# Performance work log

Measured on AMD Instinct MI355X. Metric: run time of the kernel, lower is better.

## Reference

```python
import jax, jax.numpy as jnp
import numpy as np

B, S, I = 64, 64, 20          # batch, history len, input_size
H = 1024                      # hidden_size
T = 32                        # future_seq_len
LP = 16                       # last_price_size = 4 * (I // 5)
NL = 2                        # num_layers


def setup_inputs() -> dict:
    key = jax.random.key(0)
    ks = jax.random.split(key, 14)
    s = 1.0 / np.sqrt(H)  # torch LSTM/Linear default uniform init scale
    def w(k, shape):
        return jax.random.uniform(k, shape, jnp.float32, -s, s)
    return {
        "x": jax.random.normal(ks[0], (B, S, I), jnp.float32),
        "last_price": jax.random.normal(ks[1], (B, LP), jnp.float32),
        # LSTM layer 0 (input -> hidden), gates ordered i,f,g,o as in torch
        "Wih0": w(ks[2], (4 * H, I)), "Whh0": w(ks[3], (4 * H, H)),
        "bih0": w(ks[4], (4 * H,)),   "bhh0": w(ks[5], (4 * H,)),
        # LSTM layer 1 (hidden -> hidden)
        "Wih1": w(ks[6], (4 * H, H)), "Whh1": w(ks[7], (4 * H, H)),
        "bih1": w(ks[8], (4 * H,)),   "bhh1": w(ks[9], (4 * H,)),
        # fc: Linear(H+LP -> H), ReLU, Linear(H -> I)
        "W1": w(ks[10], (H, H + LP)), "b1": w(ks[11], (H,)),
        "W2": w(ks[12], (I, H)),      "b2": w(ks[13], (I,)),
    }


def _cell(x_t, h, c, Wih, Whh, bih, bhh):
    # single LSTM cell step, torch gate order i,f,g,o
    gates = x_t @ Wih.T + h @ Whh.T + (bih + bhh)     # [B, 4H]
    i, f, g, o = jnp.split(gates, 4, axis=-1)
    c = jax.nn.sigmoid(f) * c + jax.nn.sigmoid(i) * jnp.tanh(g)
    h = jax.nn.sigmoid(o) * jnp.tanh(c)
    return h, c


def _stack_step(layers, hs, cs, inp):
    nh, nc = [], []
    for l in range(NL):
        h, c = _cell(inp, hs[l], cs[l], *layers[l])
        nh.append(h); nc.append(c)
        inp = h
    return tuple(nh), tuple(nc), inp


def _forward(x, last_price, layers, W1, b1, W2, b2):
    b = x.shape[0]
    h0 = tuple(jnp.zeros((b, H), x.dtype) for _ in range(NL))
    c0 = tuple(jnp.zeros((b, H), x.dtype) for _ in range(NL))

    def enc(carry, xt):
        hs, cs = carry
        hs, cs, _ = _stack_step(layers, hs, cs, xt)
        return (hs, cs), None

    (hs, cs), _ = jax.lax.scan(enc, (h0, c0), jnp.swapaxes(x, 0, 1))

    ngroup = I // 5  # I=20 -> %5 branch of the price update

    def dec(carry, _):
        hs, cs, cur, lp = carry
        hs, cs, top = _stack_step(layers, hs, cs, cur)
        fc_in = jnp.concatenate([top, lp], axis=1)            # [B, H+LP]
        pred = jnp.maximum(fc_in @ W1.T + b1, 0.0) @ W2.T + b2  # [B, I]
        pd = jax.lax.stop_gradient(pred)                      # torch .detach()
        # lp[:, i*4:(i+1)*4] += pd[:, i*5:i*5+4] / 100
        lp = lp + pd.reshape(b, ngroup, 5)[:, :, :4].reshape(b, ngroup * 4) / 100.0
        return (hs, cs, pd, lp), pred

    cur0 = x[:, -1, :]
    _, outs = jax.lax.scan(dec, (hs, cs, cur0, last_price), None, length=T)
    return jnp.swapaxes(outs, 0, 1)  # [B, T, I]


def reference(x, last_price, Wih0, Whh0, bih0, bhh0, Wih1, Whh1, bih1, bhh1, W1, b1, W2, b2):
    layers = [(Wih0, Whh0, bih0, bhh0), (Wih1, Whh1, bih1, bhh1)]
    return _forward(x, last_price, layers, W1, b1, W2, b2)
```

## Files before the change

### kernel.cpp

```cpp
#include <hip/hip_runtime.h>

typedef __attribute__((ext_vector_type(8))) short short8;
typedef __attribute__((ext_vector_type(4))) float float4_;
typedef unsigned long long u64;
typedef __attribute__((ext_vector_type(2))) unsigned long long u64x2;

#define AGENT __HIP_MEMORY_SCOPE_AGENT

__device__ __attribute__((aligned(4096))) unsigned long long gws_static[3702784];

__device__ __forceinline__ unsigned short f2bf(float f) {
    unsigned u = __builtin_bit_cast(unsigned, f);
    u = (u + 0x7FFFu + ((u >> 16) & 1u)) >> 16;
    return (unsigned short)u;
}
__device__ __forceinline__ float bf2f(unsigned short h) {
    unsigned u = ((unsigned)h) << 16;
    return __builtin_bit_cast(float, u);
}
__device__ __forceinline__ float sigm(float x) { return 1.0f / (1.0f + __expf(-x)); }
__device__ __forceinline__ float tanhf_(float x) {
    x = fminf(fmaxf(x, -15.0f), 15.0f);
    float e = __expf(2.0f * x);
    return (e - 1.0f) / (e + 1.0f);
}

__device__ __forceinline__ void st8_coh(unsigned short* p, unsigned long long v) {
    asm volatile("global_store_dwordx2 %0, %1, off sc0 sc1" :: "v"(p), "v"(v) : "memory");
}
__device__ __forceinline__ void st2_coh(unsigned short* p, unsigned short v) {
    asm volatile("global_store_short %0, %1, off sc0 sc1" :: "v"(p), "v"((unsigned)v) : "memory");
}

__device__ __forceinline__ void gbar_arrive(unsigned* flags, unsigned target, int blk) {
    asm volatile("s_waitcnt vmcnt(0)" ::: "memory");
    __syncthreads();
    if (threadIdx.x == 0)
        __hip_atomic_store(flags + blk * 16, target, __ATOMIC_RELAXED, AGENT);
}
__device__ __forceinline__ void gbar_wait(unsigned* flags, unsigned target) {
    while (__hip_atomic_load(flags + threadIdx.x * 16, __ATOMIC_RELAXED, AGENT) < target)
        __builtin_amdgcn_s_sleep(2);
    __syncthreads();
}
__device__ __forceinline__ void gbar(unsigned* flags, unsigned target, int blk) {
    gbar_arrive(flags, target, blk);
    gbar_wait(flags, target);
}

__device__ __forceinline__ void zero4(float4_ (&a)[4]) {
    float4_ z;
    z[0] = 0.f; z[1] = 0.f; z[2] = 0.f; z[3] = 0.f;
#pragma unroll
    for (int i = 0; i < 4; i++) a[i] = z;
}
__device__ __forceinline__ void copy4(float4_ (&d)[4], const float4_ (&s)[4]) {
#pragma unroll
    for (int i = 0; i < 4; i++) d[i] = s[i];
}

#define LD2P(dst, base, OFF) \
    asm volatile("global_load_dwordx2 %0, %1, off offset:" #OFF \
                 : "=v"(dst) : "v"(base))

#define BASES8(P, A) \
    const char* P##0 = (const char*)(A) + q * 32768 + (lane >> 4) * 1024 + (lane & 15) * 8; \
    const char* P##1 = P##0 + 4096;  const char* P##2 = P##0 + 8192; \
    const char* P##3 = P##0 + 12288; const char* P##4 = P##0 + 16384; \
    const char* P##5 = P##0 + 20480; const char* P##6 = P##0 + 24576; \
    const char* P##7 = P##0 + 28672;

#define ISSUE16P(LO, HI, LD, P, O0, O1) \
    do { LD(LO[0], P##0, O0); LD(LO[1], P##1, O0); LD(LO[2], P##2, O0); \
         LD(LO[3], P##3, O0); LD(LO[4], P##4, O0); LD(LO[5], P##5, O0); \
         LD(LO[6], P##6, O0); LD(LO[7], P##7, O0); \
         LD(HI[0], P##0, O1); LD(HI[1], P##1, O1); LD(HI[2], P##2, O1); \
         LD(HI[3], P##3, O1); LD(HI[4], P##4, O1); LD(HI[5], P##5, O1); \
         LD(HI[6], P##6, O1); LD(HI[7], P##7, O1); } while (0)

#define WAITV16(N, LO, HI) \
    asm volatile("s_waitcnt vmcnt(" #N ")" \
                 : "+v"(LO[0]), "+v"(LO[1]), "+v"(LO[2]), "+v"(LO[3]), \
                   "+v"(LO[4]), "+v"(LO[5]), "+v"(LO[6]), "+v"(LO[7]), \
                   "+v"(HI[0]), "+v"(HI[1]), "+v"(HI[2]), "+v"(HI[3]), \
                   "+v"(HI[4]), "+v"(HI[5]), "+v"(HI[6]), "+v"(HI[7]))

#define MFMA8C(LO, HI, BF, ACCI) \
    do { _Pragma("unroll") \
         for (int s_ = 0; s_ < 8; s_++) { \
             u64x2 t_; t_[0] = LO[s_]; t_[1] = HI[s_]; \
             ACCI = __builtin_amdgcn_mfma_f32_16x16x32_bf16( \
                 __builtin_bit_cast(short8, t_), BF[s_], ACCI, 0, 0, 0); } } while (0)

__device__ __forceinline__ void mm_pipe(const unsigned short* __restrict__ A,
                                        int q, int lane,
                                        const short8 (&bf)[8], float4_ (&acc)[4]) {
    BASES8(p_, A)
    u64 loA[8], hiA[8], loB[8], hiB[8];
    ISSUE16P(loA, hiA, LD2P, p_, 0, 512);
    ISSUE16P(loB, hiB, LD2P, p_, 128, 640);
    WAITV16(16, loA, hiA); MFMA8C(loA, hiA, bf, acc[0]);
    ISSUE16P(loA, hiA, LD2P, p_, 256, 768);
    WAITV16(16, loB, hiB); MFMA8C(loB, hiB, bf, acc[1]);
    ISSUE16P(loB, hiB, LD2P, p_, 384, 896);
    WAITV16(16, loA, hiA); MFMA8C(loA, hiA, bf, acc[2]);
    WAITV16(0, loB, hiB);  MFMA8C(loB, hiB, bf, acc[3]);
}

__device__ __forceinline__ void write_parts(float* gp, int q, int lane, float4_ (&acc)[4]) {
    const int col = lane & 15;
    const int rbase = (lane >> 4) * 4;
#pragma unroll
    for (int mt = 0; mt < 4; mt++)
#pragma unroll
        for (int r = 0; r < 4; r++)
            gp[(q * 64 + mt * 16 + rbase + r) * 17 + col] = acc[mt][r];
}

__device__ __forceinline__ float gsum(const float* gp, int b, int c) {
    return gp[(0 * 64 + b) * 17 + c] + gp[(1 * 64 + b) * 17 + c] +
           gp[(2 * 64 + b) * 17 + c] + gp[(3 * 64 + b) * 17 + c];
}

__device__ __forceinline__ short8 packrow(const float* __restrict__ p) {
    short8 r;
#pragma unroll
    for (int j = 0; j < 8; j++) r[j] = (short)f2bf(p[j]);
    return r;
}

__global__ void __launch_bounds__(256, 1)
lstm_core(const float* __restrict__ x, const float* __restrict__ lastp,
          const float* __restrict__ Wih0, const float* __restrict__ Whh0,
          const float* __restrict__ bih0, const float* __restrict__ bhh0,
          const float* __restrict__ Wih1, const float* __restrict__ Whh1,
          const float* __restrict__ bih1, const float* __restrict__ bhh1,
          const float* __restrict__ W1, const float* __restrict__ b1,
          const float* __restrict__ W2, const float* __restrict__ b2,
          float* __restrict__ out, unsigned char* __restrict__ wsb)
{
    const int tid = threadIdx.x;
    const int blk = blockIdx.x;
    const int lane = tid & 63;
    const int q = tid >> 6;
    const int eb = tid >> 2;
    const int eu = tid & 3;
    const int D_ = blk * 4 + eu;

    unsigned* bar   = (unsigned*)wsb;
    unsigned* flags = (unsigned*)(wsb + 8192);
    unsigned short* h0base = (unsigned short*)gws_static;
    unsigned short* h1base = h0base + (size_t)97 * 65536;
    unsigned short* relub  = h0base + (size_t)194 * 65536;

    auto h0p = [&](int g) -> unsigned short* {
        return h0base + (size_t)(g + 1) * 65536;
    };
    auto h1p = [&](int g) -> unsigned short* {
        return h1base + (size_t)(g + 1) * 65536;
    };

    __shared__ float gparts[4 * 64 * 17];
    __shared__ float xlds[2][64 * 21];
    __shared__ float wih0l[16 * 20];

    if (blk == 0) {
        __hip_atomic_store(flags + tid * 16, 0u, __ATOMIC_RELAXED, AGENT);
        __syncthreads();
        if (tid == 0)
            __hip_atomic_store(bar + 544, 0x1357BDFu, __ATOMIC_RELEASE, AGENT);
    }

    for (int i = tid; i < 1280; i += 256) {
        const int bb = i / 20, mm = i - bb * 20;
        xlds[0][bb * 21 + mm] = x[bb * 1280 + mm];
    }

    const int n_ = lane & 15;
    const int gq_ = n_ >> 2, uu_ = n_ & 3;
    const int growL = gq_ * 1024 + blk * 4 + uu_;
    const int kq = (q << 8) + ((lane >> 4) << 3);

    short8 whh0f[8], wih1f[8], whh1f[8], wfusedf[8], wfcf[8];
#pragma unroll
    for (int s = 0; s < 8; s++) {
        const int k = kq + s * 32;
        whh0f[s] = packrow(Whh0 + growL * 1024 + k);
        wih1f[s] = packrow(Wih1 + growL * 1024 + k);
        whh1f[s] = packrow(Whh1 + growL * 1024 + k);
        {
            float a8[8] = {0.f, 0.f, 0.f, 0.f, 0.f, 0.f, 0.f, 0.f};
            for (int m = 0; m < 20; m++) {
                float wv = Wih0[growL * 20 + m];
                const float* w2p = W2 + m * 1024 + k;
#pragma unroll
                for (int j = 0; j < 8; j++) a8[j] += wv * w2p[j];
            }
            short8 r;
#pragma unroll
            for (int j = 0; j < 8; j++) r[j] = (short)f2bf(a8[j]);
            wfusedf[s] = r;
        }
        {
            short8 r;
            if (n_ < 4) {
                r = packrow(W1 + (blk * 4 + n_) * 1040 + k);
            } else if (n_ < 8) {
                const int D = blk * 4 + (n_ - 4);
                float a8[8] = {0.f, 0.f, 0.f, 0.f, 0.f, 0.f, 0.f, 0.f};
                for (int g2 = 0; g2 < 16; g2++) {
                    const int m = 5 * (g2 >> 2) + (g2 & 3);
                    float wv = W1[D * 1040 + 1024 + g2] * 0.01f;
                    const float* w2p = W2 + m * 1024 + k;
#pragma unroll
                    for (int j = 0; j < 8; j++) a8[j] += wv * w2p[j];
                }
#pragma unroll
                for (int j = 0; j < 8; j++) r[j] = (short)f2bf(a8[j]);
            } else {
#pragma unroll
                for (int j = 0; j < 8; j++) r[j] = 0;
            }
            wfcf[s] = r;
        }
    }

    float bias0g[4], bias1g[4], cgv[4];
#pragma unroll
    for (int g = 0; g < 4; g++) {
        const int row = g * 1024 + D_;
        bias0g[g] = bih0[row] + bhh0[row];
        bias1g[g] = bih1[row] + bhh1[row];
        float s = 0.f;
        for (int m = 0; m < 20; m++) s += Wih0[row * 20 + m] * b2[m];
        cgv[g] = s;
    }
    const float fcb = b1[D_];
    float cbv = 0.f, ustate = 0.f;
    for (int g2 = 0; g2 < 16; g2++) {
        const float w1v = W1[D_ * 1040 + 1024 + g2];
        cbv += b2[5 * (g2 >> 2) + (g2 & 3)] * w1v * 0.01f;
        ustate += lastp[eb * 16 + g2] * w1v;
    }
    float c0v = 0.f, c1v = 0.f;

    if (tid < 16) {
        const int row = (tid >> 2) * 1024 + blk * 4 + (tid & 3);
        for (int m = 0; m < 20; m++) wih0l[tid * 20 + m] = Wih0[row * 20 + m];
    }
    if (tid < 64) {
        st8_coh(h0p(-1) + blk * 256 + tid * 4, 0ull);
        st8_coh(h1p(-1) + blk * 256 + tid * 4, 0ull);
    }

    if (tid == 0) {
        while (__hip_atomic_load(bar + 544, __ATOMIC_RELAXED, AGENT) != 0x1357BDFu)
            __builtin_amdgcn_s_sleep(2);
    }
    __syncthreads();
    unsigned tgt = 1;
    gbar(flags, tgt, blk); tgt++;

    auto publish = [&](unsigned short* dst, unsigned short val) {
        st2_coh(dst + blk * 256 + tid, val);
    };

    auto l0_finish = [&](float4_ (&acc)[4], unsigned short* h0dst, int xt, int pf) {
        write_parts(gparts, q, lane, acc);
        __syncthreads();
        if (pf >= 0) {
            for (int i = tid; i < 1280; i += 256) {
                const int bb = i / 20, mm = i - bb * 20;
                xlds[pf & 1][bb * 21 + mm] = x[bb * 1280 + pf * 20 + mm];
            }
        }
        float gv[4];
#pragma unroll
        for (int g = 0; g < 4; g++) gv[g] = gsum(gparts, eb, g * 4 + eu) + bias0g[g];
        if (xt >= 0) {
#pragma unroll
            for (int g = 0; g < 4; g++) {
                float s = 0.f;
                const float* wr = &wih0l[(g * 4 + eu) * 20];
                const float* xr = &xlds[xt & 1][eb * 21];
                for (int m = 0; m < 20; m++) s += xr[m] * wr[m];
                gv[g] += s;
            }
        } else {
#pragma unroll
            for (int g = 0; g < 4; g++) gv[g] += cgv[g];
        }
        const float iv = sigm(gv[0]), fv = sigm(gv[1]);
        const float gt = tanhf_(gv[2]), ov = sigm(gv[3]);
        c0v = fv * c0v + iv * gt;
        publish(h0dst, f2bf(ov * tanhf_(c0v)));
    };

    auto l1_finish = [&](float4_ (&acc)[4], unsigned short* h1dst) {
        write_parts(gparts, q, lane, acc);
        __syncthreads();
        float gv[4];
#pragma unroll
        for (int g = 0; g < 4; g++) gv[g] = gsum(gparts, eb, g * 4 + eu) + bias1g[g];
        const float iv = sigm(gv[0]), fv = sigm(gv[1]);
        const float gt = tanhf_(gv[2]), ov = sigm(gv[3]);
        c1v = fv * c1v + iv * gt;
        publish(h1dst, f2bf(ov * tanhf_(c1v)));
    };

    auto fc_finish = [&](int t, float4_ (&acc1)[4], float4_ (&acc2)[4]) {
        const int col = lane & 15;
        const int rbase = (lane >> 4) * 4;
        if (col < 8) {
#pragma unroll
            for (int mt = 0; mt < 4; mt++)
#pragma unroll
                for (int r = 0; r < 4; r++) {
                    const float v = (col < 4) ? acc1[mt][r] : acc2[mt][r];
                    gparts[(q * 64 + mt * 16 + rbase + r) * 17 + col] = v;
                }
        }
        __syncthreads();
        const float s1 = gsum(gparts, eb, eu);
        if (t > 0) ustate += gsum(gparts, eb, 4 + eu) + cbv;
        const float rv = fmaxf(s1 + ustate + fcb, 0.f);
        publish(relub + t * 65536, f2bf(rv));
    };

    for (int g = 0; g < 64; g++) {
        float4_ acc[4];
        zero4(acc);
        mm_pipe(h0p(g - 1), q, lane, whh0f, acc);
        l0_finish(acc, h0p(g), g, (g < 63) ? g + 1 : -1);
        gbar(flags, tgt, blk); tgt++;
        zero4(acc);
        mm_pipe(h0p(g), q, lane, wih1f, acc);
        mm_pipe(h1p(g - 1), q, lane, whh1f, acc);
        l1_finish(acc, h1p(g));
    }

    float4_ haccL0[4];
    float4_ hacc2[4];
    bool haveL0 = false;
    for (int t = 0; t < 32; t++) {
        const int g = 64 + t;
        unsigned short* rp = (t > 0) ? (relub + (t - 1) * 65536) : nullptr;

        float4_ acc[4];
        if (haveL0) {
            copy4(acc, haccL0);
        } else {
            zero4(acc);
            mm_pipe(h0p(g - 1), q, lane, whh0f, acc);
        }
        if (rp) mm_pipe(rp, q, lane, wfusedf, acc);
        l0_finish(acc, h0p(g), (t == 0) ? 63 : -1, -1);
        gbar_arrive(flags, tgt, blk);
        if (rp) {
            zero4(hacc2);
            mm_pipe(rp, q, lane, wfcf, hacc2);
        }
        gbar_wait(flags, tgt); tgt++;

        zero4(acc);
        mm_pipe(h0p(g), q, lane, wih1f, acc);
        mm_pipe(h1p(g - 1), q, lane, whh1f, acc);
        l1_finish(acc, h1p(g));
        gbar_arrive(flags, tgt, blk);
        gbar_wait(flags, tgt); tgt++;

        float4_ acc1[4], acc2[4];
        zero4(acc1);
        mm_pipe(h1p(g), q, lane, wfcf, acc1);
        if (rp) copy4(acc2, hacc2); else zero4(acc2);
        fc_finish(t, acc1, acc2);
        gbar_arrive(flags, tgt, blk);
        if (t < 31) {
            zero4(haccL0);
            mm_pipe(h0p(g), q, lane, whh0f, haccL0);
            haveL0 = true;
        }
        gbar_wait(flags, tgt); tgt++;
    }

    {
        const int pj = tid >> 5;
        const int m = tid & 31;
        if (m < 20) {
            const int pidx = blk * 8 + pj;
            const int tt = pidx >> 6, bb = pidx & 63;
            const unsigned short* rr = relub + tt * 65536;
            const float* w = W2 + m * 1024;
            float acc = 0.f;
            for (int c = 0; c < 256; c++) {
                const u64 v8 = *(const u64*)(rr + c * 256 + bb * 4);
#pragma unroll
                for (int j = 0; j < 4; j++)
                    acc += bf2f((unsigned short)(v8 >> (16 * j))) * w[c * 4 + j];
            }
            out[bb * 640 + tt * 20 + m] = acc + b2[m];
        }
    }
}

extern "C" void kernel_launch(void* const* d_in, const int* in_sizes, int n_in,
                              void* d_out, int out_size, void* d_ws, size_t ws_size,
                              hipStream_t stream) {
    (void)in_sizes; (void)n_in; (void)out_size; (void)ws_size;
    const float* x     = (const float*)d_in[0];
    const float* lastp = (const float*)d_in[1];
    const float* Wih0  = (const float*)d_in[2];
    const float* Whh0  = (const float*)d_in[3];
    const float* bih0  = (const float*)d_in[4];
    const float* bhh0  = (const float*)d_in[5];
    const float* Wih1  = (const float*)d_in[6];
    const float* Whh1  = (const float*)d_in[7];
    const float* bih1  = (const float*)d_in[8];
    const float* bhh1  = (const float*)d_in[9];
    const float* W1    = (const float*)d_in[10];
    const float* b1    = (const float*)d_in[11];
    const float* W2    = (const float*)d_in[12];
    const float* b2    = (const float*)d_in[13];
    float* out = (float*)d_out;
    unsigned char* ws = (unsigned char*)d_ws;

    void* args[] = {&x, &lastp, &Wih0, &Whh0, &bih0, &bhh0, &Wih1, &Whh1,
                    &bih1, &bhh1, &W1, &b1, &W2, &b2, &out, &ws};
    hipError_t err = hipLaunchCooperativeKernel((const void*)lstm_core,
                                                dim3(256), dim3(256), args, 0, stream);
    if (err != hipSuccess) {
        hipLaunchKernelGGL(lstm_core, dim3(256), dim3(256), 0, stream,
                           x, lastp, Wih0, Whh0, bih0, bhh0, Wih1, Whh1,
                           bih1, bhh1, W1, b1, W2, b2, out, ws);
    }
}
```

Baseline: 1.439 ms.

## Halve block count, give each block 8 hidden units with dual-B MFMA

```diff
diff --git a/kernel.cpp b/kernel.cpp
--- a/kernel.cpp
+++ b/kernel.cpp
@@ -2,8 +2,8 @@
 
 typedef __attribute__((ext_vector_type(8))) short short8;
 typedef __attribute__((ext_vector_type(4))) float float4_;
+typedef __attribute__((ext_vector_type(4))) int int4_;
 typedef unsigned long long u64;
-typedef __attribute__((ext_vector_type(2))) unsigned long long u64x2;
 
 #define AGENT __HIP_MEMORY_SCOPE_AGENT
 
@@ -28,8 +28,8 @@
 __device__ __forceinline__ void st8_coh(unsigned short* p, unsigned long long v) {
     asm volatile("global_store_dwordx2 %0, %1, off sc0 sc1" :: "v"(p), "v"(v) : "memory");
 }
-__device__ __forceinline__ void st2_coh(unsigned short* p, unsigned short v) {
-    asm volatile("global_store_short %0, %1, off sc0 sc1" :: "v"(p), "v"((unsigned)v) : "memory");
+__device__ __forceinline__ void st4_coh(unsigned short* p, unsigned v) {
+    asm volatile("global_store_dword %0, %1, off sc0 sc1" :: "v"(p), "v"(v) : "memory");
 }
 
 __device__ __forceinline__ void gbar_arrive(unsigned* flags, unsigned target, int blk) {
@@ -39,8 +39,10 @@
         __hip_atomic_store(flags + blk * 16, target, __ATOMIC_RELAXED, AGENT);
 }
 __device__ __forceinline__ void gbar_wait(unsigned* flags, unsigned target) {
-    while (__hip_atomic_load(flags + threadIdx.x * 16, __ATOMIC_RELAXED, AGENT) < target)
-        __builtin_amdgcn_s_sleep(2);
+    if (threadIdx.x < 128) {
+        while (__hip_atomic_load(flags + threadIdx.x * 16, __ATOMIC_RELAXED, AGENT) < target)
+            __builtin_amdgcn_s_sleep(2);
+    }
     __syncthreads();
 }
 __device__ __forceinline__ void gbar(unsigned* flags, unsigned target, int blk) {
@@ -54,72 +56,67 @@
 #pragma unroll
     for (int i = 0; i < 4; i++) a[i] = z;
 }
-__device__ __forceinline__ void copy4(float4_ (&d)[4], const float4_ (&s)[4]) {
-#pragma unroll
-    for (int i = 0; i < 4; i++) d[i] = s[i];
-}
-
-#define LD2P(dst, base, OFF) \
-    asm volatile("global_load_dwordx2 %0, %1, off offset:" #OFF \
+
+#define LD4P(dst, base, OFF) \
+    asm volatile("global_load_dwordx4 %0, %1, off offset:" #OFF \
                  : "=v"(dst) : "v"(base))
 
 #define BASES8(P, A) \
-    const char* P##0 = (const char*)(A) + q * 32768 + (lane >> 4) * 1024 + (lane & 15) * 8; \
+    const char* P##0 = (const char*)(A) + q * 32768 + (lane >> 4) * 1024 + (lane & 15) * 16; \
     const char* P##1 = P##0 + 4096;  const char* P##2 = P##0 + 8192; \
     const char* P##3 = P##0 + 12288; const char* P##4 = P##0 + 16384; \
     const char* P##5 = P##0 + 20480; const char* P##6 = P##0 + 24576; \
     const char* P##7 = P##0 + 28672;
 
-#define ISSUE16P(LO, HI, LD, P, O0, O1) \
-    do { LD(LO[0], P##0, O0); LD(LO[1], P##1, O0); LD(LO[2], P##2, O0); \
-         LD(LO[3], P##3, O0); LD(LO[4], P##4, O0); LD(LO[5], P##5, O0); \
-         LD(LO[6], P##6, O0); LD(LO[7], P##7, O0); \
-         LD(HI[0], P##0, O1); LD(HI[1], P##1, O1); LD(HI[2], P##2, O1); \
-         LD(HI[3], P##3, O1); LD(HI[4], P##4, O1); LD(HI[5], P##5, O1); \
-         LD(HI[6], P##6, O1); LD(HI[7], P##7, O1); } while (0)
-
-#define WAITV16(N, LO, HI) \
+#define ISSUE8(F, P, OFF) \
+    do { LD4P(F[0], P##0, OFF); LD4P(F[1], P##1, OFF); LD4P(F[2], P##2, OFF); \
+         LD4P(F[3], P##3, OFF); LD4P(F[4], P##4, OFF); LD4P(F[5], P##5, OFF); \
+         LD4P(F[6], P##6, OFF); LD4P(F[7], P##7, OFF); } while (0)
+
+#define WAITV8(N, F) \
     asm volatile("s_waitcnt vmcnt(" #N ")" \
-                 : "+v"(LO[0]), "+v"(LO[1]), "+v"(LO[2]), "+v"(LO[3]), \
-                   "+v"(LO[4]), "+v"(LO[5]), "+v"(LO[6]), "+v"(LO[7]), \
-                   "+v"(HI[0]), "+v"(HI[1]), "+v"(HI[2]), "+v"(HI[3]), \
-                   "+v"(HI[4]), "+v"(HI[5]), "+v"(HI[6]), "+v"(HI[7]))
-
-#define MFMA8C(LO, HI, BF, ACCI) \
+                 : "+v"(F[0]), "+v"(F[1]), "+v"(F[2]), "+v"(F[3]), \
+                   "+v"(F[4]), "+v"(F[5]), "+v"(F[6]), "+v"(F[7]))
+
+#define MFMA8D(F, B1, B2, A1, A2) \
     do { _Pragma("unroll") \
          for (int s_ = 0; s_ < 8; s_++) { \
-             u64x2 t_; t_[0] = LO[s_]; t_[1] = HI[s_]; \
-             ACCI = __builtin_amdgcn_mfma_f32_16x16x32_bf16( \
-                 __builtin_bit_cast(short8, t_), BF[s_], ACCI, 0, 0, 0); } } while (0)
+             short8 f_ = __builtin_bit_cast(short8, F[s_]); \
+             A1 = __builtin_amdgcn_mfma_f32_16x16x32_bf16(f_, B1[s_], A1, 0, 0, 0); \
+             A2 = __builtin_amdgcn_mfma_f32_16x16x32_bf16(f_, B2[s_], A2, 0, 0, 0); } } while (0)
 
 __device__ __forceinline__ void mm_pipe(const unsigned short* __restrict__ A,
                                         int q, int lane,
-                                        const short8 (&bf)[8], float4_ (&acc)[4]) {
+                                        const short8 (&b1)[8], const short8 (&b2)[8],
+                                        float4_ (&a1)[4], float4_ (&a2)[4]) {
     BASES8(p_, A)
-    u64 loA[8], hiA[8], loB[8], hiB[8];
-    ISSUE16P(loA, hiA, LD2P, p_, 0, 512);
-    ISSUE16P(loB, hiB, LD2P, p_, 128, 640);
-    WAITV16(16, loA, hiA); MFMA8C(loA, hiA, bf, acc[0]);
-    ISSUE16P(loA, hiA, LD2P, p_, 256, 768);
-    WAITV16(16, loB, hiB); MFMA8C(loB, hiB, bf, acc[1]);
-    ISSUE16P(loB, hiB, LD2P, p_, 384, 896);
-    WAITV16(16, loA, hiA); MFMA8C(loA, hiA, bf, acc[2]);
-    WAITV16(0, loB, hiB);  MFMA8C(loB, hiB, bf, acc[3]);
-}
-
-__device__ __forceinline__ void write_parts(float* gp, int q, int lane, float4_ (&acc)[4]) {
+    int4_ fA[8], fB[8];
+    ISSUE8(fA, p_, 0);
+    ISSUE8(fB, p_, 256);
+    WAITV8(8, fA); MFMA8D(fA, b1, b2, a1[0], a2[0]);
+    ISSUE8(fA, p_, 512);
+    WAITV8(8, fB); MFMA8D(fB, b1, b2, a1[1], a2[1]);
+    ISSUE8(fB, p_, 768);
+    WAITV8(8, fA); MFMA8D(fA, b1, b2, a1[2], a2[2]);
+    WAITV8(0, fB); MFMA8D(fB, b1, b2, a1[3], a2[3]);
+}
+
+__device__ __forceinline__ void write_parts(float* gp, int q, int lane,
+                                            float4_ (&a1)[4], float4_ (&a2)[4]) {
     const int col = lane & 15;
     const int rbase = (lane >> 4) * 4;
 #pragma unroll
     for (int mt = 0; mt < 4; mt++)
 #pragma unroll
-        for (int r = 0; r < 4; r++)
-            gp[(q * 64 + mt * 16 + rbase + r) * 17 + col] = acc[mt][r];
+        for (int r = 0; r < 4; r++) {
+            gp[(q * 64 + mt * 16 + rbase + r) * 33 + col] = a1[mt][r];
+            gp[(q * 64 + mt * 16 + rbase + r) * 33 + 16 + col] = a2[mt][r];
+        }
 }
 
 __device__ __forceinline__ float gsum(const float* gp, int b, int c) {
-    return gp[(0 * 64 + b) * 17 + c] + gp[(1 * 64 + b) * 17 + c] +
-           gp[(2 * 64 + b) * 17 + c] + gp[(3 * 64 + b) * 17 + c];
+    return gp[(0 * 64 + b) * 33 + c] + gp[(1 * 64 + b) * 33 + c] +
+           gp[(2 * 64 + b) * 33 + c] + gp[(3 * 64 + b) * 33 + c];
 }
 
 __device__ __forceinline__ short8 packrow(const float* __restrict__ p) {
@@ -145,7 +142,6 @@
     const int q = tid >> 6;
     const int eb = tid >> 2;
     const int eu = tid & 3;
-    const int D_ = blk * 4 + eu;
 
     unsigned* bar   = (unsigned*)wsb;
     unsigned* flags = (unsigned*)(wsb + 8192);
@@ -160,12 +156,13 @@
         return h1base + (size_t)(g + 1) * 65536;
     };
 
-    __shared__ float gparts[4 * 64 * 17];
+    __shared__ float gparts[4 * 64 * 33];
     __shared__ float xlds[2][64 * 21];
-    __shared__ float wih0l[16 * 20];
+    __shared__ float wih0l[32 * 20];
 
     if (blk == 0) {
-        __hip_atomic_store(flags + tid * 16, 0u, __ATOMIC_RELAXED, AGENT);
+        if (tid < 128)
+            __hip_atomic_store(flags + tid * 16, 0u, __ATOMIC_RELAXED, AGENT);
         __syncthreads();
         if (tid == 0)
             __hip_atomic_store(bar + 544, 0x1357BDFu, __ATOMIC_RELEASE, AGENT);
@@ -178,79 +175,90 @@
 
     const int n_ = lane & 15;
     const int gq_ = n_ >> 2, uu_ = n_ & 3;
-    const int growL = gq_ * 1024 + blk * 4 + uu_;
     const int kq = (q << 8) + ((lane >> 4) << 3);
 
-    short8 whh0f[8], wih1f[8], whh1f[8], wfusedf[8], wfcf[8];
-#pragma unroll
-    for (int s = 0; s < 8; s++) {
-        const int k = kq + s * 32;
-        whh0f[s] = packrow(Whh0 + growL * 1024 + k);
-        wih1f[s] = packrow(Wih1 + growL * 1024 + k);
-        whh1f[s] = packrow(Whh1 + growL * 1024 + k);
-        {
-            float a8[8] = {0.f, 0.f, 0.f, 0.f, 0.f, 0.f, 0.f, 0.f};
-            for (int m = 0; m < 20; m++) {
-                float wv = Wih0[growL * 20 + m];
-                const float* w2p = W2 + m * 1024 + k;
-#pragma unroll
-                for (int j = 0; j < 8; j++) a8[j] += wv * w2p[j];
-            }
-            short8 r;
-#pragma unroll
-            for (int j = 0; j < 8; j++) r[j] = (short)f2bf(a8[j]);
-            wfusedf[s] = r;
-        }
-        {
-            short8 r;
-            if (n_ < 4) {
-                r = packrow(W1 + (blk * 4 + n_) * 1040 + k);
-            } else if (n_ < 8) {
-                const int D = blk * 4 + (n_ - 4);
+    short8 whh0f[2][8], wih1f[2][8], whh1f[2][8], wfusedf[2][8], wfcf[2][8];
+#pragma unroll
+    for (int gr = 0; gr < 2; gr++) {
+        const int growL = gq_ * 1024 + blk * 8 + gr * 4 + uu_;
+#pragma unroll
+        for (int s = 0; s < 8; s++) {
+            const int k = kq + s * 32;
+            whh0f[gr][s] = packrow(Whh0 + growL * 1024 + k);
+            wih1f[gr][s] = packrow(Wih1 + growL * 1024 + k);
+            whh1f[gr][s] = packrow(Whh1 + growL * 1024 + k);
+            {
                 float a8[8] = {0.f, 0.f, 0.f, 0.f, 0.f, 0.f, 0.f, 0.f};
-                for (int g2 = 0; g2 < 16; g2++) {
-                    const int m = 5 * (g2 >> 2) + (g2 & 3);
-                    float wv = W1[D * 1040 + 1024 + g2] * 0.01f;
+                for (int m = 0; m < 20; m++) {
+                    float wv = Wih0[growL * 20 + m];
                     const float* w2p = W2 + m * 1024 + k;
 #pragma unroll
                     for (int j = 0; j < 8; j++) a8[j] += wv * w2p[j];
                 }
+                short8 r;
 #pragma unroll
                 for (int j = 0; j < 8; j++) r[j] = (short)f2bf(a8[j]);
-            } else {
-#pragma unroll
-                for (int j = 0; j < 8; j++) r[j] = 0;
+                wfusedf[gr][s] = r;
             }
-            wfcf[s] = r;
-        }
-    }
-
-    float bias0g[4], bias1g[4], cgv[4];
-#pragma unroll
-    for (int g = 0; g < 4; g++) {
-        const int row = g * 1024 + D_;
-        bias0g[g] = bih0[row] + bhh0[row];
-        bias1g[g] = bih1[row] + bhh1[row];
-        float s = 0.f;
-        for (int m = 0; m < 20; m++) s += Wih0[row * 20 + m] * b2[m];
-        cgv[g] = s;
-    }
-    const float fcb = b1[D_];
-    float cbv = 0.f, ustate = 0.f;
-    for (int g2 = 0; g2 < 16; g2++) {
-        const float w1v = W1[D_ * 1040 + 1024 + g2];
-        cbv += b2[5 * (g2 >> 2) + (g2 & 3)] * w1v * 0.01f;
-        ustate += lastp[eb * 16 + g2] * w1v;
-    }
-    float c0v = 0.f, c1v = 0.f;
-
-    if (tid < 16) {
-        const int row = (tid >> 2) * 1024 + blk * 4 + (tid & 3);
+            {
+                short8 r;
+                if (n_ < 4) {
+                    r = packrow(W1 + (blk * 8 + gr * 4 + n_) * 1040 + k);
+                } else if (n_ < 8) {
+                    const int D = blk * 8 + gr * 4 + (n_ - 4);
+                    float a8[8] = {0.f, 0.f, 0.f, 0.f, 0.f, 0.f, 0.f, 0.f};
+                    for (int g2 = 0; g2 < 16; g2++) {
+                        const int m = 5 * (g2 >> 2) + (g2 & 3);
+                        float wv = W1[D * 1040 + 1024 + g2] * 0.01f;
+                        const float* w2p = W2 + m * 1024 + k;
+#pragma unroll
+                        for (int j = 0; j < 8; j++) a8[j] += wv * w2p[j];
+                    }
+#pragma unroll
+                    for (int j = 0; j < 8; j++) r[j] = (short)f2bf(a8[j]);
+                } else {
+#pragma unroll
+                    for (int j = 0; j < 8; j++) r[j] = 0;
+                }
+                wfcf[gr][s] = r;
+            }
+        }
+    }
+
+    float bias0g[2][4], bias1g[2][4], cgv[2][4];
+    float fcb[2], cbv[2], ustate[2], c0v[2], c1v[2];
+#pragma unroll
+    for (int ui = 0; ui < 2; ui++) {
+        const int D_ = blk * 8 + 2 * eu + ui;
+#pragma unroll
+        for (int g = 0; g < 4; g++) {
+            const int row = g * 1024 + D_;
+            bias0g[ui][g] = bih0[row] + bhh0[row];
+            bias1g[ui][g] = bih1[row] + bhh1[row];
+            float s = 0.f;
+            for (int m = 0; m < 20; m++) s += Wih0[row * 20 + m] * b2[m];
+            cgv[ui][g] = s;
+        }
+        fcb[ui] = b1[D_];
+        float cb = 0.f, us = 0.f;
+        for (int g2 = 0; g2 < 16; g2++) {
+            const float w1v = W1[D_ * 1040 + 1024 + g2];
+            cb += b2[5 * (g2 >> 2) + (g2 & 3)] * w1v * 0.01f;
+            us += lastp[eb * 16 + g2] * w1v;
+        }
+        cbv[ui] = cb;
+        ustate[ui] = us;
+        c0v[ui] = 0.f;
+        c1v[ui] = 0.f;
+    }
+
+    if (tid < 32) {
+        const int row = (tid >> 3) * 1024 + blk * 8 + (tid & 7);
         for (int m = 0; m < 20; m++) wih0l[tid * 20 + m] = Wih0[row * 20 + m];
     }
-    if (tid < 64) {
-        st8_coh(h0p(-1) + blk * 256 + tid * 4, 0ull);
-        st8_coh(h1p(-1) + blk * 256 + tid * 4, 0ull);
+    if (tid < 128) {
+        st8_coh(h0p(-1) + blk * 512 + tid * 4, 0ull);
+        st8_coh(h1p(-1) + blk * 512 + tid * 4, 0ull);
     }
 
     if (tid == 0) {
@@ -261,12 +269,14 @@
     unsigned tgt = 1;
     gbar(flags, tgt, blk); tgt++;
 
-    auto publish = [&](unsigned short* dst, unsigned short val) {
-        st2_coh(dst + blk * 256 + tid, val);
-    };
-
-    auto l0_finish = [&](float4_ (&acc)[4], unsigned short* h0dst, int xt, int pf) {
-        write_parts(gparts, q, lane, acc);
+    auto publish = [&](unsigned short* dst, unsigned short v0, unsigned short v1) {
+        st4_coh(dst + blk * 512 + eb * 8 + eu * 2,
+                (unsigned)v0 | ((unsigned)v1 << 16));
+    };
+
+    auto l0_finish = [&](float4_ (&a1)[4], float4_ (&a2)[4],
+                         unsigned short* h0dst, int xt, int pf) {
+        write_parts(gparts, q, lane, a1, a2);
         __syncthreads();
         if (pf >= 0) {
             for (int i = tid; i < 1280; i += 256) {
@@ -274,129 +284,140 @@
                 xlds[pf & 1][bb * 21 + mm] = x[bb * 1280 + pf * 20 + mm];
             }
         }
-        float gv[4];
-#pragma unroll
-        for (int g = 0; g < 4; g++) gv[g] = gsum(gparts, eb, g * 4 + eu) + bias0g[g];
-        if (xt >= 0) {
-#pragma unroll
-            for (int g = 0; g < 4; g++) {
-                float s = 0.f;
-                const float* wr = &wih0l[(g * 4 + eu) * 20];
-                const float* xr = &xlds[xt & 1][eb * 21];
-                for (int m = 0; m < 20; m++) s += xr[m] * wr[m];
-                gv[g] += s;
+        unsigned short hv[2];
+#pragma unroll
+        for (int ui = 0; ui < 2; ui++) {
+            const int u = 2 * eu + ui;
+            const int cb_ = (u >> 2) * 16 + (u & 3);
+            float gv[4];
+#pragma unroll
+            for (int g = 0; g < 4; g++) gv[g] = gsum(gparts, eb, cb_ + g * 4) + bias0g[ui][g];
+            if (xt >= 0) {
+#pragma unroll
+                for (int g = 0; g < 4; g++) {
+                    float s = 0.f;
+                    const float* wr = &wih0l[(g * 8 + u) * 20];
+                    const float* xr = &xlds[xt & 1][eb * 21];
+                    for (int m = 0; m < 20; m++) s += xr[m] * wr[m];
+                    gv[g] += s;
+                }
+            } else {
+#pragma unroll
+                for (int g = 0; g < 4; g++) gv[g] += cgv[ui][g];
             }
-        } else {
-#pragma unroll
-            for (int g = 0; g < 4; g++) gv[g] += cgv[g];
-        }
-        const float iv = sigm(gv[0]), fv = sigm(gv[1]);
-        const float gt = tanhf_(gv[2]), ov = sigm(gv[3]);
-        c0v = fv * c0v + iv * gt;
-        publish(h0dst, f2bf(ov * tanhf_(c0v)));
-    };
-
-    auto l1_finish = [&](float4_ (&acc)[4], unsigned short* h1dst) {
-        write_parts(gparts, q, lane, acc);
+            const float iv = sigm(gv[0]), fv = sigm(gv[1]);
+            const float gt = tanhf_(gv[2]), ov = sigm(gv[3]);
+            c0v[ui] = fv * c0v[ui] + iv * gt;
+            hv[ui] = f2bf(ov * tanhf_(c0v[ui]));
+        }
+        publish(h0dst, hv[0], hv[1]);
+    };
+
+    auto l1_finish = [&](float4_ (&a1)[4], float4_ (&a2)[4], unsigned short* h1dst) {
+        write_parts(gparts, q, lane, a1, a2);
         __syncthreads();
-        float gv[4];
-#pragma unroll
-        for (int g = 0; g < 4; g++) gv[g] = gsum(gparts, eb, g * 4 + eu) + bias1g[g];
-        const float iv = sigm(gv[0]), fv = sigm(gv[1]);
-        const float gt = tanhf_(gv[2]), ov = sigm(gv[3]);
-        c1v = fv * c1v + iv * gt;
-        publish(h1dst, f2bf(ov * tanhf_(c1v)));
-    };
-
-    auto fc_finish = [&](int t, float4_ (&acc1)[4], float4_ (&acc2)[4]) {
+        unsigned short hv[2];
+#pragma unroll
+        for (int ui = 0; ui < 2; ui++) {
+            const int u = 2 * eu + ui;
+            const int cb_ = (u >> 2) * 16 + (u & 3);
+            float gv[4];
+#pragma unroll
+            for (int g = 0; g < 4; g++) gv[g] = gsum(gparts, eb, cb_ + g * 4) + bias1g[ui][g];
+            const float iv = sigm(gv[0]), fv = sigm(gv[1]);
+            const float gt = tanhf_(gv[2]), ov = sigm(gv[3]);
+            c1v[ui] = fv * c1v[ui] + iv * gt;
+            hv[ui] = f2bf(ov * tanhf_(c1v[ui]));
+        }
+        publish(h1dst, hv[0], hv[1]);
+    };
+
+    auto fc_write = [&](float4_ (&a1)[4], float4_ (&a2)[4], int cofs) {
         const int col = lane & 15;
         const int rbase = (lane >> 4) * 4;
-        if (col < 8) {
+        if ((col & ~3) == cofs) {
 #pragma unroll
             for (int mt = 0; mt < 4; mt++)
 #pragma unroll
                 for (int r = 0; r < 4; r++) {
-                    const float v = (col < 4) ? acc1[mt][r] : acc2[mt][r];
-                    gparts[(q * 64 + mt * 16 + rbase + r) * 17 + col] = v;
+                    gparts[(q * 64 + mt * 16 + rbase + r) * 33 + col] = a1[mt][r];
+                    gparts[(q * 64 + mt * 16 + rbase + r) * 33 + 16 + col] = a2[mt][r];
                 }
         }
+    };
+
+    auto fc_finish = [&](int t) {
         __syncthreads();
-        const float s1 = gsum(gparts, eb, eu);
-        if (t > 0) ustate += gsum(gparts, eb, 4 + eu) + cbv;
-        const float rv = fmaxf(s1 + ustate + fcb, 0.f);
-        publish(relub + t * 65536, f2bf(rv));
+        unsigned short rv2[2];
+#pragma unroll
+        for (int ui = 0; ui < 2; ui++) {
+            const int u = 2 * eu + ui;
+            const int cb_ = (u >> 2) * 16 + (u & 3);
+            const float s1 = gsum(gparts, eb, cb_);
+            if (t > 0) ustate[ui] += gsum(gparts, eb, cb_ + 4) + cbv[ui];
+            rv2[ui] = f2bf(fmaxf(s1 + ustate[ui] + fcb[ui], 0.f));
+        }
+        publish(relub + t * 65536, rv2[0], rv2[1]);
     };
 
     for (int g = 0; g < 64; g++) {
-        float4_ acc[4];
-        zero4(acc);
-        mm_pipe(h0p(g - 1), q, lane, whh0f, acc);
-        l0_finish(acc, h0p(g), g, (g < 63) ? g + 1 : -1);
+        float4_ a1[4], a2[4];
+        zero4(a1); zero4(a2);
+        mm_pipe(h0p(g - 1), q, lane, whh0f[0], whh0f[1], a1, a2);
+        l0_finish(a1, a2, h0p(g), g, (g < 63) ? g + 1 : -1);
         gbar(flags, tgt, blk); tgt++;
-        zero4(acc);
-        mm_pipe(h0p(g), q, lane, wih1f, acc);
-        mm_pipe(h1p(g - 1), q, lane, whh1f, acc);
-        l1_finish(acc, h1p(g));
-    }
-
-    float4_ haccL0[4];
-    float4_ hacc2[4];
-    bool haveL0 = false;
+        zero4(a1); zero4(a2);
+        mm_pipe(h0p(g), q, lane, wih1f[0], wih1f[1], a1, a2);
+        mm_pipe(h1p(g - 1), q, lane, whh1f[0], whh1f[1], a1, a2);
+        l1_finish(a1, a2, h1p(g));
+    }
+
     for (int t = 0; t < 32; t++) {
         const int g = 64 + t;
         unsigned short* rp = (t > 0) ? (relub + (t - 1) * 65536) : nullptr;
 
-        float4_ acc[4];
-        if (haveL0) {
-            copy4(acc, haccL0);
-        } else {
-            zero4(acc);
-            mm_pipe(h0p(g - 1), q, lane, whh0f, acc);
-        }
-        if (rp) mm_pipe(rp, q, lane, wfusedf, acc);
-        l0_finish(acc, h0p(g), (t == 0) ? 63 : -1, -1);
-        gbar_arrive(flags, tgt, blk);
+        float4_ a1[4], a2[4];
+        zero4(a1); zero4(a2);
+        mm_pipe(h0p(g - 1), q, lane, whh0f[0], whh0f[1], a1, a2);
+        if (rp) mm_pipe(rp, q, lane, wfusedf[0], wfusedf[1], a1, a2);
+        l0_finish(a1, a2, h0p(g), (t == 0) ? 63 : -1, -1);
+        gbar(flags, tgt, blk); tgt++;
+
+        zero4(a1); zero4(a2);
+        mm_pipe(h0p(g), q, lane, wih1f[0], wih1f[1], a1, a2);
+        mm_pipe(h1p(g - 1), q, lane, whh1f[0], whh1f[1], a1, a2);
+        l1_finish(a1, a2, h1p(g));
+        gbar(flags, tgt, blk); tgt++;
+
+        zero4(a1); zero4(a2);
+        mm_pipe(h1p(g), q, lane, wfcf[0], wfcf[1], a1, a2);
+        fc_write(a1, a2, 0);
         if (rp) {
-            zero4(hacc2);
-            mm_pipe(rp, q, lane, wfcf, hacc2);
-        }
-        gbar_wait(flags, tgt); tgt++;
-
-        zero4(acc);
-        mm_pipe(h0p(g), q, lane, wih1f, acc);
-        mm_pipe(h1p(g - 1), q, lane, whh1f, acc);
-        l1_finish(acc, h1p(g));
-        gbar_arrive(flags, tgt, blk);
-        gbar_wait(flags, tgt); tgt++;
-
-        float4_ acc1[4], acc2[4];
-        zero4(acc1);
-        mm_pipe(h1p(g), q, lane, wfcf, acc1);
-        if (rp) copy4(acc2, hacc2); else zero4(acc2);
-        fc_finish(t, acc1, acc2);
-        gbar_arrive(flags, tgt, blk);
-        if (t < 31) {
-            zero4(haccL0);
-            mm_pipe(h0p(g), q, lane, whh0f, haccL0);
-            haveL0 = true;
-        }
-        gbar_wait(flags, tgt); tgt++;
-    }
-
-    {
+            zero4(a1); zero4(a2);
+            mm_pipe(rp, q, lane, wfcf[0], wfcf[1], a1, a2);
+            fc_write(a1, a2, 4);
+        }
+        fc_finish(t);
+        gbar(flags, tgt, blk); tgt++;
+    }
+
+    for (int it = 0; it < 2; it++) {
         const int pj = tid >> 5;
         const int m = tid & 31;
         if (m < 20) {
-            const int pidx = blk * 8 + pj;
+            const int pidx = blk * 16 + it * 8 + pj;
             const int tt = pidx >> 6, bb = pidx & 63;
             const unsigned short* rr = relub + tt * 65536;
             const float* w = W2 + m * 1024;
             float acc = 0.f;
-            for (int c = 0; c < 256; c++) {
-                const u64 v8 = *(const u64*)(rr + c * 256 + bb * 4);
-#pragma unroll
-                for (int j = 0; j < 4; j++)
-                    acc += bf2f((unsigned short)(v8 >> (16 * j))) * w[c * 4 + j];
+            for (int c = 0; c < 128; c++) {
+                const u64 v0 = *(const u64*)(rr + c * 512 + bb * 8);
+                const u64 v1 = *(const u64*)(rr + c * 512 + bb * 8 + 4);
+#pragma unroll
+                for (int j = 0; j < 4; j++) {
+                    acc += bf2f((unsigned short)(v0 >> (16 * j))) * w[c * 8 + j];
+                    acc += bf2f((unsigned short)(v1 >> (16 * j))) * w[c * 8 + 4 + j];
+                }
             }
             out[bb * 640 + tt * 20 + m] = acc + b2[m];
         }
@@ -427,9 +448,9 @@
     void* args[] = {&x, &lastp, &Wih0, &Whh0, &bih0, &bhh0, &Wih1, &Whh1,
                     &bih1, &bhh1, &W1, &b1, &W2, &b2, &out, &ws};
     hipError_t err = hipLaunchCooperativeKernel((const void*)lstm_core,
-                                                dim3(256), dim3(256), args, 0, stream);
+                                                dim3(128), dim3(256), args, 0, stream);
     if (err != hipSuccess) {
-        hipLaunchKernelGGL(lstm_core, dim3(256), dim3(256), 0, stream,
+        hipLaunchKernelGGL(lstm_core, dim3(128), dim3(256), 0, stream,
                            x, lastp, Wih0, Whh0, bih0, bhh0, Wih1, Whh1,
                            bih1, bhh1, W1, b1, W2, b2, out, ws);
     }
```

New measurement: 1.987 ms. +38.1%, slower.

## Share h0 loads between layer-1 input and next-step layer-0 recurrent matmuls

Applied to the files above, without the earlier changes.

```diff
diff --git a/kernel.cpp b/kernel.cpp
--- a/kernel.cpp
+++ b/kernel.cpp
@@ -91,6 +91,14 @@
              u64x2 t_; t_[0] = LO[s_]; t_[1] = HI[s_]; \
              ACCI = __builtin_amdgcn_mfma_f32_16x16x32_bf16( \
                  __builtin_bit_cast(short8, t_), BF[s_], ACCI, 0, 0, 0); } } while (0)
+
+#define MFMA8C2(LO, HI, B1, B2, A1, A2) \
+    do { _Pragma("unroll") \
+         for (int s_ = 0; s_ < 8; s_++) { \
+             u64x2 t_; t_[0] = LO[s_]; t_[1] = HI[s_]; \
+             short8 f_ = __builtin_bit_cast(short8, t_); \
+             A1 = __builtin_amdgcn_mfma_f32_16x16x32_bf16(f_, B1[s_], A1, 0, 0, 0); \
+             A2 = __builtin_amdgcn_mfma_f32_16x16x32_bf16(f_, B2[s_], A2, 0, 0, 0); } } while (0)
 
 __device__ __forceinline__ void mm_pipe(const unsigned short* __restrict__ A,
                                         int q, int lane,
@@ -105,6 +113,22 @@
     ISSUE16P(loB, hiB, LD2P, p_, 384, 896);
     WAITV16(16, loA, hiA); MFMA8C(loA, hiA, bf, acc[2]);
     WAITV16(0, loB, hiB);  MFMA8C(loB, hiB, bf, acc[3]);
+}
+
+__device__ __forceinline__ void mm_pipe_d(const unsigned short* __restrict__ A,
+                                          int q, int lane,
+                                          const short8 (&b1)[8], const short8 (&b2)[8],
+                                          float4_ (&a1)[4], float4_ (&a2)[4]) {
+    BASES8(p_, A)
+    u64 loA[8], hiA[8], loB[8], hiB[8];
+    ISSUE16P(loA, hiA, LD2P, p_, 0, 512);
+    ISSUE16P(loB, hiB, LD2P, p_, 128, 640);
+    WAITV16(16, loA, hiA); MFMA8C2(loA, hiA, b1, b2, a1[0], a2[0]);
+    ISSUE16P(loA, hiA, LD2P, p_, 256, 768);
+    WAITV16(16, loB, hiB); MFMA8C2(loB, hiB, b1, b2, a1[1], a2[1]);
+    ISSUE16P(loB, hiB, LD2P, p_, 384, 896);
+    WAITV16(16, loA, hiA); MFMA8C2(loA, hiA, b1, b2, a1[2], a2[2]);
+    WAITV16(0, loB, hiB);  MFMA8C2(loB, hiB, b1, b2, a1[3], a2[3]);
 }
 
 __device__ __forceinline__ void write_parts(float* gp, int q, int lane, float4_ (&acc)[4]) {
@@ -327,60 +351,45 @@
         publish(relub + t * 65536, f2bf(rv));
     };
 
+    float4_ haccL0[4];
+    float4_ haccSkip[4];
+    zero4(haccL0);
+
     for (int g = 0; g < 64; g++) {
         float4_ acc[4];
-        zero4(acc);
-        mm_pipe(h0p(g - 1), q, lane, whh0f, acc);
+        copy4(acc, haccL0);
         l0_finish(acc, h0p(g), g, (g < 63) ? g + 1 : -1);
         gbar(flags, tgt, blk); tgt++;
-        zero4(acc);
-        mm_pipe(h0p(g), q, lane, wih1f, acc);
-        mm_pipe(h1p(g - 1), q, lane, whh1f, acc);
-        l1_finish(acc, h1p(g));
-    }
-
-    float4_ haccL0[4];
-    float4_ hacc2[4];
-    bool haveL0 = false;
+        float4_ accn[4];
+        zero4(accn); zero4(haccL0);
+        mm_pipe_d(h0p(g), q, lane, wih1f, whh0f, accn, haccL0);
+        mm_pipe(h1p(g - 1), q, lane, whh1f, accn);
+        l1_finish(accn, h1p(g));
+    }
+
     for (int t = 0; t < 32; t++) {
         const int g = 64 + t;
         unsigned short* rp = (t > 0) ? (relub + (t - 1) * 65536) : nullptr;
 
         float4_ acc[4];
-        if (haveL0) {
-            copy4(acc, haccL0);
-        } else {
-            zero4(acc);
-            mm_pipe(h0p(g - 1), q, lane, whh0f, acc);
-        }
-        if (rp) mm_pipe(rp, q, lane, wfusedf, acc);
+        copy4(acc, haccL0);
+        zero4(haccSkip);
+        if (rp) mm_pipe_d(rp, q, lane, wfusedf, wfcf, acc, haccSkip);
         l0_finish(acc, h0p(g), (t == 0) ? 63 : -1, -1);
-        gbar_arrive(flags, tgt, blk);
-        if (rp) {
-            zero4(hacc2);
-            mm_pipe(rp, q, lane, wfcf, hacc2);
-        }
-        gbar_wait(flags, tgt); tgt++;
-
-        zero4(acc);
-        mm_pipe(h0p(g), q, lane, wih1f, acc);
-        mm_pipe(h1p(g - 1), q, lane, whh1f, acc);
-        l1_finish(acc, h1p(g));
-        gbar_arrive(flags, tgt, blk);
-        gbar_wait(flags, tgt); tgt++;
-
-        float4_ acc1[4], acc2[4];
+        gbar(flags, tgt, blk); tgt++;
+
+        float4_ accn[4];
+        zero4(accn); zero4(haccL0);
+        mm_pipe_d(h0p(g), q, lane, wih1f, whh0f, accn, haccL0);
+        mm_pipe(h1p(g - 1), q, lane, whh1f, accn);
+        l1_finish(accn, h1p(g));
+        gbar(flags, tgt, blk); tgt++;
+
+        float4_ acc1[4];
         zero4(acc1);
         mm_pipe(h1p(g), q, lane, wfcf, acc1);
-        if (rp) copy4(acc2, hacc2); else zero4(acc2);
-        fc_finish(t, acc1, acc2);
-        gbar_arrive(flags, tgt, blk);
-        if (t < 31) {
-            zero4(haccL0);
-            mm_pipe(h0p(g), q, lane, whh0f, haccL0);
-            haveL0 = true;
-        }
-        gbar_wait(flags, tgt); tgt++;
+        fc_finish(t, acc1, haccSkip);
+        gbar(flags, tgt, blk); tgt++;
     }
 
     {
```

After: 1.246 ms. -13.4%, faster.
